# Kernel tuning notes

Measured on AMD Instinct MI355X. Metric: run time of the kernel, lower is better.

The kernel has to match this reference:

```python
import jax, jax.numpy as jnp
import numpy as np
import math

# ---- cfg constants (PUMA functional model defaults) ----
XBAR_ROW, XBAR_COL = 128, 128
GON, GOFF, VMAX = 1.0 / 100.0, 1.0 / 600.0, 0.25  # cancel exactly in ideal ADC decode
BIT_SLICE, BIT_STREAM = 2, 1
WEIGHT_BITS, INPUT_BITS = 16, 16
W_FRAC = WEIGHT_BITS // 4 * 3   # 12 fractional bits (default -1 path)
I_FRAC = INPUT_BITS // 4 * 3    # 12
ACM_BITS = 16
ACM_FRAC = ACM_BITS // 4 * 3    # 12 -> accumulator range [-8, 8)
ADC_BIT = int(math.log2(XBAR_ROW)) + BIT_SLICE  # 7 + 2 = 9 (bit_stream==1 adds nothing)
NSLICE = 2 ** BIT_SLICE - 1     # conductance states per slice
NS = WEIGHT_BITS // BIT_SLICE   # 8 weight slices, MSB first
NB = INPUT_BITS // BIT_STREAM   # 16 input bit streams, LSB first


def bit_slicing(w):
    # w: [out, in] nonnegative -> [in, out*NS]; per output col, NS slices MSB first
    wint = jnp.clip(jnp.round(w * 2.0 ** W_FRAC), 0.0, 2.0 ** WEIGHT_BITS - 1)
    shifts = 2.0 ** (BIT_SLICE * jnp.arange(NS - 1, -1, -1, dtype=jnp.float32))
    sl = jnp.floor(wint[:, :, None] / shifts) % (2 ** BIT_SLICE)  # [out,in,NS]
    return sl.transpose(1, 0, 2).reshape(w.shape[1], w.shape[0] * NS)


def to_bits(x):
    # two's-complement fixed-point bits, LSB first -> [B, in, NB]
    xint = jnp.clip(jnp.round(x * 2.0 ** I_FRAC), -(2.0 ** (INPUT_BITS - 1)), 2.0 ** (INPUT_BITS - 1) - 1)
    xint = jnp.where(xint < 0, xint + 2.0 ** INPUT_BITS, xint)
    shifts = 2.0 ** jnp.arange(INPUT_BITS, dtype=jnp.float32)
    return jnp.floor(xint[:, :, None] / shifts) % 2.0


def tile(ws, rt, ct):
    # pad [rows, cols] to crossbar tiles [rt, ct, XBAR_ROW, XBAR_COL]
    pad = jnp.zeros((rt * XBAR_ROW, ct * XBAR_COL), ws.dtype)
    pad = pad.at[:ws.shape[0], :ws.shape[1]].set(ws)
    return pad.reshape(rt, XBAR_ROW, ct, XBAR_COL).transpose(0, 2, 1, 3)


def quant_acm(v):
    lim = 2.0 ** (ACM_BITS - ACM_FRAC - 1)
    q = jnp.round(v * 2.0 ** ACM_FRAC) / 2.0 ** ACM_FRAC
    return jnp.clip(q, -lim, lim - 2.0 ** (-ACM_FRAC))


def crossbar_mvm(bits, slices):
    # bits: [B, R, 128, NB] in {0,1}; slices: [R, C, 128, 128] in {0..NSLICE}
    G = slices * (GON - GOFF) / NSLICE + GOFF          # conductance mapping
    V = bits * VMAX                                     # DAC (1-bit streams)
    # analog column currents per stream: [B, R, C, NB, 128]
    I = jnp.einsum('brks,rckj->brcsj', V, G)
    vsum = V.sum(2)                                     # [B, R, NB]
    # ideal decode: remove Goff offset, rescale to integer dot counts
    counts = (I - vsum[:, :, None, :, None] * GOFF) / (VMAX * (GON - GOFF) / NSLICE)
    # ADC quantization over full-scale range xbar_row*NSLICE with 2**ADC_BIT levels
    step = (XBAR_ROW * NSLICE) / (2.0 ** ADC_BIT - 1)
    counts = jnp.round(counts / step) * step
    B, R, C = counts.shape[:3]
    counts = counts.reshape(B, R, C, NB, XBAR_COL // NS, NS)
    slice_w = 2.0 ** (BIT_SLICE * jnp.arange(NS - 1, -1, -1, dtype=jnp.float32))
    psum = (counts * slice_w).sum(-1)                   # shift-add slices -> [B,R,C,NB,cols]
    stream_w = 2.0 ** jnp.arange(NB, dtype=jnp.float32)
    stream_w = stream_w.at[-1].multiply(-1.0)           # two's-complement MSB is negative
    out = (psum * stream_w[:, None]).sum(3)             # shift-add streams -> [B,R,C,cols]
    out = quant_acm(out / 2.0 ** (W_FRAC + I_FRAC))     # back to float, accumulator quant
    out = out.sum(1)                                    # digital sum over row tiles
    return out.reshape(B, C * (XBAR_COL // NS))


def mvm_forward(x, weight):
    out_f, in_f = weight.shape
    pos = bit_slicing(jnp.clip(weight, 0.0, None))
    neg = bit_slicing(jnp.abs(jnp.clip(weight, None, 0.0)))
    rt = -(-pos.shape[0] // XBAR_ROW)
    ct = -(-pos.shape[1] // XBAR_COL)
    xb_pos, xb_neg = tile(pos, rt, ct), tile(neg, rt, ct)
    bits = to_bits(x)                                   # [B, in, NB]
    B = x.shape[0]
    bits_p = jnp.zeros((B, rt * XBAR_ROW, NB), x.dtype).at[:, :in_f].set(bits)
    bits_p = bits_p.reshape(B, rt, XBAR_ROW, NB)
    out = crossbar_mvm(bits_p, xb_pos) - crossbar_mvm(bits_p, xb_neg)
    return out[:, :out_f]


def setup_inputs() -> dict:
    key = jax.random.key(0)
    k1, k2, k3 = jax.random.split(key, 3)
    x = jax.random.normal(k1, (512, 1024), dtype=jnp.float32) * 0.1
    weight = jax.random.normal(k2, (128, 1024), dtype=jnp.float32) * 0.05
    bias = jax.random.uniform(k3, (128,), dtype=jnp.float32, minval=-0.1, maxval=0.1)
    return {"x": x, "weight": weight, "bias": bias}


def reference(x, weight, bias):
    return mvm_forward(x, weight) + bias[None, :]
```

## Files before the change

kernel.cpp:

```cpp
#include <hip/hip_runtime.h>
#include <stdint.h>

typedef __attribute__((ext_vector_type(4)))  int i32x4;
typedef __attribute__((ext_vector_type(16))) int i32x16;

#define XM_OFF 0u
#define BP_OFF 1048576u
#define MK_OFF 3145728u
#define DT_OFF 3149824u

__device__ __forceinline__ uint32_t q16(float v){
  float f = fminf(fmaxf(rintf(v*4096.f), -32768.f), 32767.f);
  return (uint32_t)(int)f & 0xffffu;
}

__global__ __launch_bounds__(256) void pack_k(const float* __restrict__ x, const float* __restrict__ w,
                                              const float* __restrict__ bias,
                                              uint4* __restrict__ xm, uint32_t* __restrict__ Bw,
                                              uint16_t* __restrict__ mk, uint8_t* __restrict__ dirty,
                                              float* __restrict__ out){
  const int lane = threadIdx.x & 63;
  if (blockIdx.x < 1024){
    int wv = blockIdx.x*4 + (threadIdx.x >> 6);
    int b = wv >> 3, z = wv & 7;
    const float* xp = x + b*1024 + z*128;
    uint32_t u0 = q16(xp[lane]);
    uint32_t u1 = q16(xp[lane + 64]);
    uint32_t v0 = ((u0 - 2048u) & 0xFFFFu) < 61440u;
    uint32_t v1 = ((u1 - 2048u) & 0xFFFFu) < 61440u;
    unsigned long long bal = __ballot(v0 != 0u) | __ballot(v1 != 0u);
    if (lane == 0) dirty[z*512 + b] = (bal != 0ull) ? 1u : 0u;
    uint4 out4 = {0,0,0,0};
    #pragma unroll
    for (int s = 0; s < 16; ++s){
      unsigned long long m0 = __ballot((u0 >> s) & 1u);
      unsigned long long m1 = __ballot((u1 >> s) & 1u);
      if (lane == s){
        out4.x = (uint32_t)m0; out4.y = (uint32_t)(m0 >> 32);
        out4.z = (uint32_t)m1; out4.w = (uint32_t)(m1 >> 32);
      }
    }
    if (lane < 16) xm[(b*8 + z)*16 + lane] = out4;
  } else if (blockIdx.x < 1152){
    int t = (blockIdx.x - 1024)*256 + threadIdx.x;
    int j = t >> 8, kq = t & 255;
    int r = kq >> 5, kd = kq & 31;
    float4 v = *reinterpret_cast<const float4*>(w + j*1024 + kq*4);
    uint32_t lm = 0;
    #pragma unroll
    for (int p = 0; p < 2; ++p){
      uint32_t q0 = (uint32_t)fminf(rintf(fmaxf(p ? -v.x : v.x, 0.f)*4096.f), 65535.f);
      uint32_t q1 = (uint32_t)fminf(rintf(fmaxf(p ? -v.y : v.y, 0.f)*4096.f), 65535.f);
      uint32_t q2 = (uint32_t)fminf(rintf(fmaxf(p ? -v.z : v.z, 0.f)*4096.f), 65535.f);
      uint32_t q3 = (uint32_t)fminf(rintf(fmaxf(p ? -v.w : v.w, 0.f)*4096.f), 65535.f);
      #pragma unroll
      for (int sl = 0; sl < 8; ++sl){
        int sh = 2*(7 - sl);
        uint32_t word = ((q0 >> sh) & 3u) | (((q1 >> sh) & 3u) << 8)
                      | (((q2 >> sh) & 3u) << 16) | (((q3 >> sh) & 3u) << 24);
        Bw[(((r*2 + p)*8 + sl)*128 + j)*32 + kd] = word;
        lm |= (word != 0u ? 1u : 0u) << (p*8 + sl);
      }
    }
    lm |= (uint32_t)__shfl_xor((int)lm, 16);
    lm |= (uint32_t)__shfl_xor((int)lm, 8);
    lm |= (uint32_t)__shfl_xor((int)lm, 4);
    lm |= (uint32_t)__shfl_xor((int)lm, 2);
    lm |= (uint32_t)__shfl_xor((int)lm, 1);
    if ((threadIdx.x & 31) == 0) mk[r*128 + j] = (uint16_t)lm;
  } else {
    int t = (blockIdx.x - 1152)*256 + threadIdx.x;
    out[t] = rintf(bias[t & 127]*4096.f)*(1.0f/4096.0f);
  }
}

__global__ __launch_bounds__(512, 4) void mvm_all_k(const uint4* __restrict__ xm,
                                                    const uint8_t* __restrict__ Bp,
                                                    const uint16_t* __restrict__ mk,
                                                    const uint8_t* __restrict__ dirty,
                                                    float* __restrict__ out){
  __shared__ uint8_t lds[13*4096];
  const int tid = threadIdx.x, lane = tid & 63, wid = tid >> 6;
  const int jblk = blockIdx.y, z = blockIdx.z;
  const int col = lane & 31, hi = lane >> 5;
  const float C1 = (float)(511.0/384.0);
  const float QC = (float)(384.0/511.0/4096.0);

  uint32_t mv = ((const uint32_t*)mk)[z*64 + jblk*16 + (lane & 15)];
  mv |= (uint32_t)__shfl_xor((int)mv, 1);
  mv |= (uint32_t)__shfl_xor((int)mv, 2);
  mv |= (uint32_t)__shfl_xor((int)mv, 4);
  mv |= (uint32_t)__shfl_xor((int)mv, 8);
  const uint32_t msk = (uint32_t)__builtin_amdgcn_readfirstlane((int)((mv | (mv >> 16)) & 0xFFFFu));

  if (blockIdx.x >= 32){
    const int fx = blockIdx.x - 32;
    const int p  = fx >> 3;
    const int bb64 = (fx & 7)*64;
    const int bg = bb64 + wid*8;
    const uint64_t d8 = *(const uint64_t*)(dirty + z*512 + bg);
    const uint32_t mbits = (msk >> (p*8)) & 0xFFu;

    if (mbits & (1u << wid)){
      const int q = lane >> 3, cS = (lane & 7) ^ q;
      const uint8_t* src = Bp + ((size_t)((z*16 + p*8 + wid)*128 + jblk*32) << 7);
      uint4 r0 = *(const uint4*)(src + (q     )*128 + cS*16);
      uint4 r1 = *(const uint4*)(src + (q +  8)*128 + cS*16);
      uint4 r2 = *(const uint4*)(src + (q + 16)*128 + cS*16);
      uint4 r3 = *(const uint4*)(src + (q + 24)*128 + cS*16);
      uint8_t* dst = lds + wid*4096 + lane*16;
      *(uint4*)(dst       ) = r0;
      *(uint4*)(dst + 1024) = r1;
      *(uint4*)(dst + 2048) = r2;
      *(uint4*)(dst + 3072) = r3;
    }
    __syncthreads();
    if (d8 != 0ull) return;

    const int s_loc = lane & 3;
    const int b_loc = (lane & 31) >> 2;
    i32x4 afr0[4], afr1[4], afr2[4];
    {
      const size_t xb = ((size_t)(bg + b_loc)*8 + z)*16;
      const uint4 p0 = xm[xb + s_loc];
      const uint4 p1 = xm[xb + 4 + s_loc];
      const uint4 p2 = xm[xb + ((s_loc == 3) ? 15 : (8 + s_loc))];
      const uint32_t w0[4] = {p0.x, p0.y, p0.z, p0.w};
      const uint32_t w1[4] = {p1.x, p1.y, p1.z, p1.w};
      const uint32_t w2[4] = {p2.x, p2.y, p2.z, p2.w};
      #pragma unroll
      for (int f = 0; f < 4; ++f){
        uint32_t a = w0[f] >> (hi*16), b = w1[f] >> (hi*16), c = w2[f] >> (hi*16);
        #pragma unroll
        for (int wI = 0; wI < 4; ++wI){
          afr0[f][wI] = (int)((((a >> (wI*4)) & 0xFu) * 0x204081u) & 0x01010101u);
          afr1[f][wI] = (int)((((b >> (wI*4)) & 0xFu) * 0x204081u) & 0x01010101u);
          afr2[f][wI] = (int)((((c >> (wI*4)) & 0xFu) * 0x204081u) & 0x01010101u);
        }
      }
    }

    const int c7 = col & 7;
    const int xo0 = ((0 + hi) ^ c7) << 4;
    const int xo1 = ((2 + hi) ^ c7) << 4;
    const int xo2 = ((4 + hi) ^ c7) << 4;
    const int xo3 = ((6 + hi) ^ c7) << 4;
    i32x16 zz;
    #pragma unroll
    for (int i = 0; i < 16; ++i) zz[i] = 0;

    float acc[4] = {0.f, 0.f, 0.f, 0.f};

#define EPIF(cc, w3v, gsl) do { \
    _Pragma("unroll") \
    for (int q_ = 0; q_ < 4; ++q_){ \
      float n0 = rintf((float)cc[q_*4+0]*C1), n1 = rintf((float)cc[q_*4+1]*C1); \
      float n2 = rintf((float)cc[q_*4+2]*C1), n3 = rintf((float)cc[q_*4+3]*C1); \
      float t = fmaf(n1, 2.f, n0); t = fmaf(n2, 4.f, t); t = fmaf(n3, (w3v), t); \
      acc[q_] = fmaf(t, (gsl), acc[q_]); \
    } \
  } while (0)
#define CHAIN(cc, A) do { \
    cc = __builtin_amdgcn_mfma_i32_32x32x32_i8(A[0], b0, zz, 0, 0, 0); \
    cc = __builtin_amdgcn_mfma_i32_32x32x32_i8(A[1], b1, cc, 0, 0, 0); \
    cc = __builtin_amdgcn_mfma_i32_32x32x32_i8(A[2], b2, cc, 0, 0, 0); \
    cc = __builtin_amdgcn_mfma_i32_32x32x32_i8(A[3], b3, cc, 0, 0, 0); \
  } while (0)

    #pragma unroll
    for (int sl = 0; sl < 8; ++sl){
      if (mbits & (1u << sl)){
        const float slwv = (float)(1 << (14 - 2*sl));
        const uint8_t* lb = lds + sl*4096 + col*128;
        i32x4 b0 = *(const i32x4*)(lb + xo0);
        i32x4 b1 = *(const i32x4*)(lb + xo1);
        i32x4 b2 = *(const i32x4*)(lb + xo2);
        i32x4 b3 = *(const i32x4*)(lb + xo3);
        i32x16 cc0, cc1, cc2;
        CHAIN(cc0, afr0);
        CHAIN(cc1, afr1);
        EPIF(cc0, 8.f, slwv);
        CHAIN(cc2, afr2);
        EPIF(cc1, 8.f, slwv*16.f);
        EPIF(cc2, -8.f, slwv*256.f);
      }
    }
#undef CHAIN
#undef EPIF

    const float sgn = p ? -1.f : 1.f;
    const int jout = jblk*32 + col;
    #pragma unroll
    for (int q_ = 0; q_ < 4; ++q_){
      float qv = fminf(fmaxf(rintf(acc[q_]*QC)*(1.0f/4096.0f), -8.0f), 8.0f - 1.0f/4096.0f);
      atomicAdd(&out[(bg + 2*q_ + hi)*128 + jout], sgn*qv);
    }
    return;
  }

  const int bbB = blockIdx.x*16;
  const uint64_t dA = *(const uint64_t*)(dirty + z*512 + bbB);
  const uint64_t dB = *(const uint64_t*)(dirty + z*512 + bbB + 8);
  if ((dA | dB) == 0ull) return;

  {
    const int q = lane >> 3, cS = (lane & 7) ^ q;
    int slot = 0;
    #pragma unroll
    for (int ti = 0; ti < 16; ++ti){
      if (msk & (1u << ti)){
        if ((slot == wid || slot == wid + 8) && slot < 13){
          const uint8_t* src = Bp + ((size_t)((z*16 + ti)*128 + jblk*32) << 7);
          uint4 r0 = *(const uint4*)(src + (q     )*128 + cS*16);
          uint4 r1 = *(const uint4*)(src + (q +  8)*128 + cS*16);
          uint4 r2 = *(const uint4*)(src + (q + 16)*128 + cS*16);
          uint4 r3 = *(const uint4*)(src + (q + 24)*128 + cS*16);
          uint8_t* dst = lds + slot*4096 + lane*16;
          *(uint4*)(dst       ) = r0;
          *(uint4*)(dst + 1024) = r1;
          *(uint4*)(dst + 2048) = r2;
          *(uint4*)(dst + 3072) = r3;
        }
        ++slot;
      }
    }
  }
  __syncthreads();

  const int bb = bbB + wid*2;
  const bool active = (wid < 4) ? (dA != 0ull) : (dB != 0ull);
  if (!active) return;

  const int s_a = lane & 15;
  const uint4 pw = xm[((size_t)(bb + (col >> 4))*8 + z)*16 + s_a];
  i32x4 afr[4];
  {
    const uint32_t wd[4] = {pw.x, pw.y, pw.z, pw.w};
    #pragma unroll
    for (int f = 0; f < 4; ++f){
      uint32_t pl = wd[f] >> (hi*16);
      #pragma unroll
      for (int wI = 0; wI < 4; ++wI)
        afr[f][wI] = (int)((((pl >> (wI*4)) & 0xFu) * 0x204081u) & 0x01010101u);
    }
  }

  const int c7 = col & 7;
  const int xo0 = ((0 + hi) ^ c7) << 4;
  const int xo1 = ((2 + hi) ^ c7) << 4;
  const int xo2 = ((4 + hi) ^ c7) << 4;
  const int xo3 = ((6 + hi) ^ c7) << 4;
  i32x16 zz;
  #pragma unroll
  for (int i = 0; i < 16; ++i) zz[i] = 0;

  const float sc = hi ? 16.0f : 1.0f;
  const float w7 = hi ? -8.0f : 8.0f;
  float a00 = 0.f, a01 = 0.f, a10 = 0.f, a11 = 0.f;

#define EPIS(cc, A0, A1) do { \
    float nf[16]; \
    _Pragma("unroll") \
    for (int g_ = 0; g_ < 16; ++g_) nf[g_] = rintf((float)cc[g_] * C1); \
    float t0 = fmaf(nf[1], 2.f, nf[0]);  t0 = fmaf(nf[2], 4.f, t0);  t0 = fmaf(nf[3], 8.f, t0); \
    float t1 = fmaf(nf[5], 2.f, nf[4]);  t1 = fmaf(nf[6], 4.f, t1);  t1 = fmaf(nf[7], w7, t1); \
    float t2 = fmaf(nf[9], 2.f, nf[8]);  t2 = fmaf(nf[10],4.f, t2);  t2 = fmaf(nf[11],8.f, t2); \
    float t3 = fmaf(nf[13],2.f, nf[12]); t3 = fmaf(nf[14],4.f, t3);  t3 = fmaf(nf[15],w7, t3); \
    A0 = fmaf(t0, slwv, A0);  A0 = fmaf(t1, slw256, A0); \
    A1 = fmaf(t2, slwv, A1);  A1 = fmaf(t3, slw256, A1); \
  } while (0)

  {
    int slot2 = 0;
    #pragma unroll
    for (int ti = 0; ti < 16; ++ti){
      if (msk & (1u << ti)){
        const int sl = ti & 7;
        const float slwv   = (float)(1 << (14 - 2*sl));
        const float slw256 = slwv * 256.0f;
        i32x4 b0, b1, b2, b3;
        if (slot2 < 13){
          const uint8_t* lb = lds + slot2*4096 + col*128;
          b0 = *(const i32x4*)(lb + xo0);
          b1 = *(const i32x4*)(lb + xo1);
          b2 = *(const i32x4*)(lb + xo2);
          b3 = *(const i32x4*)(lb + xo3);
        } else {
          const uint8_t* gb = Bp + ((size_t)((z*16 + ti)*128 + jblk*32 + col) << 7) + hi*16;
          b0 = *(const i32x4*)(gb      );
          b1 = *(const i32x4*)(gb + 32 );
          b2 = *(const i32x4*)(gb + 64 );
          b3 = *(const i32x4*)(gb + 96 );
        }
        i32x16 cc = __builtin_amdgcn_mfma_i32_32x32x32_i8(afr[0], b0, zz, 0, 0, 0);
        cc = __builtin_amdgcn_mfma_i32_32x32x32_i8(afr[1], b1, cc, 0, 0, 0);
        cc = __builtin_amdgcn_mfma_i32_32x32x32_i8(afr[2], b2, cc, 0, 0, 0);
        cc = __builtin_amdgcn_mfma_i32_32x32x32_i8(afr[3], b3, cc, 0, 0, 0);
        if (ti < 8) EPIS(cc, a00, a01);
        else        EPIS(cc, a10, a11);
        ++slot2;
      }
    }
  }
#undef EPIS

  a00 *= sc; a01 *= sc; a10 *= sc; a11 *= sc;
  a00 += __shfl_xor(a00, 32); a01 += __shfl_xor(a01, 32);
  a10 += __shfl_xor(a10, 32); a11 += __shfl_xor(a11, 32);
  float q00 = fminf(fmaxf(rintf(a00*QC)*(1.0f/4096.0f), -8.0f), 8.0f - 1.0f/4096.0f);
  float q01 = fminf(fmaxf(rintf(a01*QC)*(1.0f/4096.0f), -8.0f), 8.0f - 1.0f/4096.0f);
  float q10 = fminf(fmaxf(rintf(a10*QC)*(1.0f/4096.0f), -8.0f), 8.0f - 1.0f/4096.0f);
  float q11 = fminf(fmaxf(rintf(a11*QC)*(1.0f/4096.0f), -8.0f), 8.0f - 1.0f/4096.0f);
  const int jout = jblk*32 + col;
  atomicAdd(&out[(bb + hi)*128 + jout], hi ? (q01 - q11) : (q00 - q10));
}

extern "C" void kernel_launch(void* const* d_in, const int* in_sizes, int n_in,
                              void* d_out, int out_size, void* d_ws, size_t ws_size,
                              hipStream_t stream){
  const float* x    = (const float*)d_in[0];
  const float* w    = (const float*)d_in[1];
  const float* bias = (const float*)d_in[2];
  uint8_t* ws = (uint8_t*)d_ws;
  float* out = (float*)d_out;

  hipLaunchKernelGGL(pack_k, dim3(1408), dim3(256), 0, stream,
                     x, w, bias, (uint4*)(ws + XM_OFF), (uint32_t*)(ws + BP_OFF),
                     (uint16_t*)(ws + MK_OFF), ws + DT_OFF, out);
  hipLaunchKernelGGL(mvm_all_k, dim3(48, 4, 8), dim3(512), 0, stream,
                     (const uint4*)(ws + XM_OFF), ws + BP_OFF,
                     (const uint16_t*)(ws + MK_OFF), ws + DT_OFF, out);
}
```

Baseline: 26.64 us.

## Stage all 16 weight slices in LDS and merge pos/neg fast-path blocks

Grows the LDS buffer to hold all 16 weight-slice tiles (positive and negative), so the slow path no longer falls back to global loads past 13 slots. The fast path now handles both polarities in one block, which halves its grid share (48 to 40 blocks in x), avoids loading the activation fragments twice, and halves the number of atomics per output. The cost is a 64KB LDS footprint that lowers the launch-bounds occupancy hint from 4 to 2 blocks, and every block now loads all slices, including clean-path blocks that then exit.

```diff
diff --git a/kernel.cpp b/kernel.cpp
--- a/kernel.cpp
+++ b/kernel.cpp
@@ -74,17 +74,18 @@
   }
 }
 
-__global__ __launch_bounds__(512, 4) void mvm_all_k(const uint4* __restrict__ xm,
+__global__ __launch_bounds__(512, 2) void mvm_all_k(const uint4* __restrict__ xm,
                                                     const uint8_t* __restrict__ Bp,
                                                     const uint16_t* __restrict__ mk,
                                                     const uint8_t* __restrict__ dirty,
                                                     float* __restrict__ out){
-  __shared__ uint8_t lds[13*4096];
+  __shared__ uint8_t lds[65536];
   const int tid = threadIdx.x, lane = tid & 63, wid = tid >> 6;
   const int jblk = blockIdx.y, z = blockIdx.z;
   const int col = lane & 31, hi = lane >> 5;
   const float C1 = (float)(511.0/384.0);
   const float QC = (float)(384.0/511.0/4096.0);
+  const bool fastrole = (blockIdx.x < 8);
 
   uint32_t mv = ((const uint32_t*)mk)[z*64 + jblk*16 + (lane & 15)];
   mv |= (uint32_t)__shfl_xor((int)mv, 1);
@@ -93,32 +94,51 @@
   mv |= (uint32_t)__shfl_xor((int)mv, 8);
   const uint32_t msk = (uint32_t)__builtin_amdgcn_readfirstlane((int)((mv | (mv >> 16)) & 0xFFFFu));
 
-  if (blockIdx.x >= 32){
-    const int fx = blockIdx.x - 32;
-    const int p  = fx >> 3;
-    const int bb64 = (fx & 7)*64;
-    const int bg = bb64 + wid*8;
+  uint64_t dA = 0ull, dB = 0ull;
+  if (!fastrole){
+    const int bbB = (blockIdx.x - 8)*16;
+    dA = *(const uint64_t*)(dirty + z*512 + bbB);
+    dB = *(const uint64_t*)(dirty + z*512 + bbB + 8);
+    if ((dA | dB) == 0ull) return;
+  }
+
+  {
+    const int q = lane >> 3, cS = (lane & 7) ^ q;
+    #pragma unroll
+    for (int u = 0; u < 2; ++u){
+      const int si = wid + u*8;
+      if (msk & (1u << si)){
+        const uint8_t* src = Bp + ((size_t)((z*16 + si)*128 + jblk*32) << 7);
+        uint4 r0 = *(const uint4*)(src + (q     )*128 + cS*16);
+        uint4 r1 = *(const uint4*)(src + (q +  8)*128 + cS*16);
+        uint4 r2 = *(const uint4*)(src + (q + 16)*128 + cS*16);
+        uint4 r3 = *(const uint4*)(src + (q + 24)*128 + cS*16);
+        uint8_t* dst = lds + si*4096 + lane*16;
+        *(uint4*)(dst       ) = r0;
+        *(uint4*)(dst + 1024) = r1;
+        *(uint4*)(dst + 2048) = r2;
+        *(uint4*)(dst + 3072) = r3;
+      }
+    }
+  }
+  __syncthreads();
+
+  const int c7 = col & 7;
+  const int xo0 = ((0 + hi) ^ c7) << 4;
+  const int xo1 = ((2 + hi) ^ c7) << 4;
+  const int xo2 = ((4 + hi) ^ c7) << 4;
+  const int xo3 = ((6 + hi) ^ c7) << 4;
+  i32x16 zz;
+  #pragma unroll
+  for (int i = 0; i < 16; ++i) zz[i] = 0;
+  const int jout = jblk*32 + col;
+
+  if (fastrole){
+    const int bg = blockIdx.x*64 + wid*8;
     const uint64_t d8 = *(const uint64_t*)(dirty + z*512 + bg);
-    const uint32_t mbits = (msk >> (p*8)) & 0xFFu;
-
-    if (mbits & (1u << wid)){
-      const int q = lane >> 3, cS = (lane & 7) ^ q;
-      const uint8_t* src = Bp + ((size_t)((z*16 + p*8 + wid)*128 + jblk*32) << 7);
-      uint4 r0 = *(const uint4*)(src + (q     )*128 + cS*16);
-      uint4 r1 = *(const uint4*)(src + (q +  8)*128 + cS*16);
-      uint4 r2 = *(const uint4*)(src + (q + 16)*128 + cS*16);
-      uint4 r3 = *(const uint4*)(src + (q + 24)*128 + cS*16);
-      uint8_t* dst = lds + wid*4096 + lane*16;
-      *(uint4*)(dst       ) = r0;
-      *(uint4*)(dst + 1024) = r1;
-      *(uint4*)(dst + 2048) = r2;
-      *(uint4*)(dst + 3072) = r3;
-    }
-    __syncthreads();
     if (d8 != 0ull) return;
 
-    const int s_loc = lane & 3;
-    const int b_loc = (lane & 31) >> 2;
+    const int s_loc = lane & 3, b_loc = col >> 2;
     i32x4 afr0[4], afr1[4], afr2[4];
     {
       const size_t xb = ((size_t)(bg + b_loc)*8 + z)*16;
@@ -140,93 +160,63 @@
       }
     }
 
-    const int c7 = col & 7;
-    const int xo0 = ((0 + hi) ^ c7) << 4;
-    const int xo1 = ((2 + hi) ^ c7) << 4;
-    const int xo2 = ((4 + hi) ^ c7) << 4;
-    const int xo3 = ((6 + hi) ^ c7) << 4;
-    i32x16 zz;
-    #pragma unroll
-    for (int i = 0; i < 16; ++i) zz[i] = 0;
-
-    float acc[4] = {0.f, 0.f, 0.f, 0.f};
-
-#define EPIF(cc, w3v, gsl) do { \
-    _Pragma("unroll") \
-    for (int q_ = 0; q_ < 4; ++q_){ \
-      float n0 = rintf((float)cc[q_*4+0]*C1), n1 = rintf((float)cc[q_*4+1]*C1); \
-      float n2 = rintf((float)cc[q_*4+2]*C1), n3 = rintf((float)cc[q_*4+3]*C1); \
-      float t = fmaf(n1, 2.f, n0); t = fmaf(n2, 4.f, t); t = fmaf(n3, (w3v), t); \
-      acc[q_] = fmaf(t, (gsl), acc[q_]); \
-    } \
-  } while (0)
 #define CHAIN(cc, A) do { \
     cc = __builtin_amdgcn_mfma_i32_32x32x32_i8(A[0], b0, zz, 0, 0, 0); \
     cc = __builtin_amdgcn_mfma_i32_32x32x32_i8(A[1], b1, cc, 0, 0, 0); \
     cc = __builtin_amdgcn_mfma_i32_32x32x32_i8(A[2], b2, cc, 0, 0, 0); \
     cc = __builtin_amdgcn_mfma_i32_32x32x32_i8(A[3], b3, cc, 0, 0, 0); \
   } while (0)
-
-    #pragma unroll
-    for (int sl = 0; sl < 8; ++sl){
-      if (mbits & (1u << sl)){
-        const float slwv = (float)(1 << (14 - 2*sl));
-        const uint8_t* lb = lds + sl*4096 + col*128;
-        i32x4 b0 = *(const i32x4*)(lb + xo0);
-        i32x4 b1 = *(const i32x4*)(lb + xo1);
-        i32x4 b2 = *(const i32x4*)(lb + xo2);
-        i32x4 b3 = *(const i32x4*)(lb + xo3);
-        i32x16 cc0, cc1, cc2;
-        CHAIN(cc0, afr0);
-        CHAIN(cc1, afr1);
-        EPIF(cc0, 8.f, slwv);
-        CHAIN(cc2, afr2);
-        EPIF(cc1, 8.f, slwv*16.f);
-        EPIF(cc2, -8.f, slwv*256.f);
-      }
-    }
+#define EPIF(cc, w3v, gsl, ACC) do { \
+    _Pragma("unroll") \
+    for (int q_ = 0; q_ < 4; ++q_){ \
+      float n0 = rintf((float)cc[q_*4+0]*C1), n1 = rintf((float)cc[q_*4+1]*C1); \
+      float n2 = rintf((float)cc[q_*4+2]*C1), n3 = rintf((float)cc[q_*4+3]*C1); \
+      float t = fmaf(n1, 2.f, n0); t = fmaf(n2, 4.f, t); t = fmaf(n3, (w3v), t); \
+      ACC[q_] = fmaf(t, (gsl), ACC[q_]); \
+    } \
+  } while (0)
+#define PBODY(p_, ACC) do { \
+    const uint32_t mb = (msk >> ((p_)*8)) & 0xFFu; \
+    _Pragma("unroll") \
+    for (int sl = 0; sl < 8; ++sl){ \
+      if (mb & (1u << sl)){ \
+        const float slwv = (float)(1 << (14 - 2*sl)); \
+        const uint8_t* lb = lds + (size_t)((p_)*8 + sl)*4096 + col*128; \
+        i32x4 b0 = *(const i32x4*)(lb + xo0); \
+        i32x4 b1 = *(const i32x4*)(lb + xo1); \
+        i32x4 b2 = *(const i32x4*)(lb + xo2); \
+        i32x4 b3 = *(const i32x4*)(lb + xo3); \
+        i32x16 cc0, cc1, cc2; \
+        CHAIN(cc0, afr0); \
+        CHAIN(cc1, afr1); \
+        EPIF(cc0, 8.f, slwv, ACC); \
+        CHAIN(cc2, afr2); \
+        EPIF(cc1, 8.f, slwv*16.f, ACC); \
+        EPIF(cc2, -8.f, slwv*256.f, ACC); \
+      } \
+    } \
+  } while (0)
+
+    float acc0[4] = {0.f, 0.f, 0.f, 0.f};
+    PBODY(0, acc0);
+    float qv0[4];
+    #pragma unroll
+    for (int q_ = 0; q_ < 4; ++q_)
+      qv0[q_] = fminf(fmaxf(rintf(acc0[q_]*QC)*(1.0f/4096.0f), -8.0f), 8.0f - 1.0f/4096.0f);
+    float acc1[4] = {0.f, 0.f, 0.f, 0.f};
+    PBODY(1, acc1);
+    #pragma unroll
+    for (int q_ = 0; q_ < 4; ++q_){
+      float qv1 = fminf(fmaxf(rintf(acc1[q_]*QC)*(1.0f/4096.0f), -8.0f), 8.0f - 1.0f/4096.0f);
+      atomicAdd(&out[(bg + 2*q_ + hi)*128 + jout], qv0[q_] - qv1);
+    }
+#undef PBODY
+#undef EPIF
 #undef CHAIN
-#undef EPIF
-
-    const float sgn = p ? -1.f : 1.f;
-    const int jout = jblk*32 + col;
-    #pragma unroll
-    for (int q_ = 0; q_ < 4; ++q_){
-      float qv = fminf(fmaxf(rintf(acc[q_]*QC)*(1.0f/4096.0f), -8.0f), 8.0f - 1.0f/4096.0f);
-      atomicAdd(&out[(bg + 2*q_ + hi)*128 + jout], sgn*qv);
-    }
     return;
   }
 
-  const int bbB = blockIdx.x*16;
-  const uint64_t dA = *(const uint64_t*)(dirty + z*512 + bbB);
-  const uint64_t dB = *(const uint64_t*)(dirty + z*512 + bbB + 8);
-  if ((dA | dB) == 0ull) return;
-
-  {
-    const int q = lane >> 3, cS = (lane & 7) ^ q;
-    int slot = 0;
-    #pragma unroll
-    for (int ti = 0; ti < 16; ++ti){
-      if (msk & (1u << ti)){
-        if ((slot == wid || slot == wid + 8) && slot < 13){
-          const uint8_t* src = Bp + ((size_t)((z*16 + ti)*128 + jblk*32) << 7);
-          uint4 r0 = *(const uint4*)(src + (q     )*128 + cS*16);
-          uint4 r1 = *(const uint4*)(src + (q +  8)*128 + cS*16);
-          uint4 r2 = *(const uint4*)(src + (q + 16)*128 + cS*16);
-          uint4 r3 = *(const uint4*)(src + (q + 24)*128 + cS*16);
-          uint8_t* dst = lds + slot*4096 + lane*16;
-          *(uint4*)(dst       ) = r0;
-          *(uint4*)(dst + 1024) = r1;
-          *(uint4*)(dst + 2048) = r2;
-          *(uint4*)(dst + 3072) = r3;
-        }
-        ++slot;
-      }
-    }
-  }
-  __syncthreads();
-
+  const int bbB = (blockIdx.x - 8)*16;
   const int bb = bbB + wid*2;
   const bool active = (wid < 4) ? (dA != 0ull) : (dB != 0ull);
   if (!active) return;
@@ -244,15 +234,6 @@
         afr[f][wI] = (int)((((pl >> (wI*4)) & 0xFu) * 0x204081u) & 0x01010101u);
     }
   }
-
-  const int c7 = col & 7;
-  const int xo0 = ((0 + hi) ^ c7) << 4;
-  const int xo1 = ((2 + hi) ^ c7) << 4;
-  const int xo2 = ((4 + hi) ^ c7) << 4;
-  const int xo3 = ((6 + hi) ^ c7) << 4;
-  i32x16 zz;
-  #pragma unroll
-  for (int i = 0; i < 16; ++i) zz[i] = 0;
 
   const float sc = hi ? 16.0f : 1.0f;
   const float w7 = hi ? -8.0f : 8.0f;
@@ -270,36 +251,23 @@
     A1 = fmaf(t2, slwv, A1);  A1 = fmaf(t3, slw256, A1); \
   } while (0)
 
-  {
-    int slot2 = 0;
-    #pragma unroll
-    for (int ti = 0; ti < 16; ++ti){
-      if (msk & (1u << ti)){
-        const int sl = ti & 7;
-        const float slwv   = (float)(1 << (14 - 2*sl));
-        const float slw256 = slwv * 256.0f;
-        i32x4 b0, b1, b2, b3;
-        if (slot2 < 13){
-          const uint8_t* lb = lds + slot2*4096 + col*128;
-          b0 = *(const i32x4*)(lb + xo0);
-          b1 = *(const i32x4*)(lb + xo1);
-          b2 = *(const i32x4*)(lb + xo2);
-          b3 = *(const i32x4*)(lb + xo3);
-        } else {
-          const uint8_t* gb = Bp + ((size_t)((z*16 + ti)*128 + jblk*32 + col) << 7) + hi*16;
-          b0 = *(const i32x4*)(gb      );
-          b1 = *(const i32x4*)(gb + 32 );
-          b2 = *(const i32x4*)(gb + 64 );
-          b3 = *(const i32x4*)(gb + 96 );
-        }
-        i32x16 cc = __builtin_amdgcn_mfma_i32_32x32x32_i8(afr[0], b0, zz, 0, 0, 0);
-        cc = __builtin_amdgcn_mfma_i32_32x32x32_i8(afr[1], b1, cc, 0, 0, 0);
-        cc = __builtin_amdgcn_mfma_i32_32x32x32_i8(afr[2], b2, cc, 0, 0, 0);
-        cc = __builtin_amdgcn_mfma_i32_32x32x32_i8(afr[3], b3, cc, 0, 0, 0);
-        if (ti < 8) EPIS(cc, a00, a01);
-        else        EPIS(cc, a10, a11);
-        ++slot2;
-      }
+  #pragma unroll
+  for (int ti = 0; ti < 16; ++ti){
+    if (msk & (1u << ti)){
+      const int sl = ti & 7;
+      const float slwv   = (float)(1 << (14 - 2*sl));
+      const float slw256 = slwv * 256.0f;
+      const uint8_t* lb = lds + (size_t)ti*4096 + col*128;
+      i32x4 b0 = *(const i32x4*)(lb + xo0);
+      i32x4 b1 = *(const i32x4*)(lb + xo1);
+      i32x4 b2 = *(const i32x4*)(lb + xo2);
+      i32x4 b3 = *(const i32x4*)(lb + xo3);
+      i32x16 cc = __builtin_amdgcn_mfma_i32_32x32x32_i8(afr[0], b0, zz, 0, 0, 0);
+      cc = __builtin_amdgcn_mfma_i32_32x32x32_i8(afr[1], b1, cc, 0, 0, 0);
+      cc = __builtin_amdgcn_mfma_i32_32x32x32_i8(afr[2], b2, cc, 0, 0, 0);
+      cc = __builtin_amdgcn_mfma_i32_32x32x32_i8(afr[3], b3, cc, 0, 0, 0);
+      if (ti < 8) EPIS(cc, a00, a01);
+      else        EPIS(cc, a10, a11);
     }
   }
 #undef EPIS
@@ -311,7 +279,6 @@
   float q01 = fminf(fmaxf(rintf(a01*QC)*(1.0f/4096.0f), -8.0f), 8.0f - 1.0f/4096.0f);
   float q10 = fminf(fmaxf(rintf(a10*QC)*(1.0f/4096.0f), -8.0f), 8.0f - 1.0f/4096.0f);
   float q11 = fminf(fmaxf(rintf(a11*QC)*(1.0f/4096.0f), -8.0f), 8.0f - 1.0f/4096.0f);
-  const int jout = jblk*32 + col;
   atomicAdd(&out[(bb + hi)*128 + jout], hi ? (q01 - q11) : (q00 - q10));
 }
 
@@ -327,7 +294,7 @@
   hipLaunchKernelGGL(pack_k, dim3(1408), dim3(256), 0, stream,
                      x, w, bias, (uint4*)(ws + XM_OFF), (uint32_t*)(ws + BP_OFF),
                      (uint16_t*)(ws + MK_OFF), ws + DT_OFF, out);
-  hipLaunchKernelGGL(mvm_all_k, dim3(48, 4, 8), dim3(512), 0, stream,
+  hipLaunchKernelGGL(mvm_all_k, dim3(40, 4, 8), dim3(512), 0, stream,
                      (const uint4*)(ws + XM_OFF), ws + BP_OFF,
                      (const uint16_t*)(ws + MK_OFF), ws + DT_OFF, out);
 }
```

New measurement: 29.51 us. 1.11x slower.
